# Kernel tuning notes

Measured on AMD Instinct MI355X. Metric: run time of the kernel, lower is better.

Reference implementation:

```python
import jax, jax.numpy as jnp
import numpy as np

N_NODES = 1_000_000
D_FEAT = 128
N_GRAPHS = 4096


def setup_inputs() -> dict:
    key = jax.random.key(0)
    k1, k2 = jax.random.split(key)
    feat = jax.random.normal(k1, (N_NODES, D_FEAT), dtype=jnp.float32)
    # per-node graph id (batched graph membership), sorted as in dgl.batch ordering
    segment_ids = jnp.sort(jax.random.randint(k2, (N_NODES,), 0, N_GRAPHS, dtype=jnp.int32))
    return {"feat": feat, "segment_ids": segment_ids, "num_segments": N_GRAPHS}


def reference(feat, segment_ids, num_segments):
    # Sum node features within each graph: [total_nodes, d] -> [num_graphs, d]
    return jax.ops.segment_sum(feat, segment_ids, num_segments=num_segments,
                               indices_are_sorted=True)
```

## Files before the change

### kernel.cpp

```cpp
#include <hip/hip_runtime.h>


#define D_FEAT 128
#define D4     32

typedef float f32x4 __attribute__((ext_vector_type(4)));

__global__ __launch_bounds__(256) void seg_offsets_kernel(
        const int* __restrict__ ids,
        int* __restrict__ offsets,
        int n_nodes, int num_segs) {
    int i = blockIdx.x * blockDim.x + threadIdx.x;
    if (i >= n_nodes) return;
    int cur  = ids[i];
    int prev = (i == 0) ? -1 : ids[i - 1];
    for (int s = prev + 1; s <= cur; ++s) offsets[s] = i;
    if (i == n_nodes - 1) {
        for (int s = cur + 1; s <= num_segs; ++s) offsets[s] = n_nodes;
    }
}

__global__ __launch_bounds__(256) void SumNode_11905649344609_kernel(
        const float* __restrict__ feat,
        const int* __restrict__ offsets,
        float* __restrict__ out) {
    const int seg   = blockIdx.x;
    const int start = offsets[seg];
    const int end   = offsets[seg + 1];

    const int tid  = threadIdx.x;
    const int c4   = tid & (D4 - 1);
    const int roff = tid >> 5;

    const f32x4* __restrict__ f4 = (const f32x4*)feat;

    f32x4 a0 = {0.f, 0.f, 0.f, 0.f};
    f32x4 a1 = a0, a2 = a0, a3 = a0;

    int r = start + roff;
    for (; r + 24 < end; r += 32) {
        f32x4 v0 = __builtin_nontemporal_load(&f4[(size_t)(r)      * D4 + c4]);
        f32x4 v1 = __builtin_nontemporal_load(&f4[(size_t)(r +  8) * D4 + c4]);
        f32x4 v2 = __builtin_nontemporal_load(&f4[(size_t)(r + 16) * D4 + c4]);
        f32x4 v3 = __builtin_nontemporal_load(&f4[(size_t)(r + 24) * D4 + c4]);
        a0 += v0; a1 += v1; a2 += v2; a3 += v3;
    }
    for (; r < end; r += 8) {
        a0 += __builtin_nontemporal_load(&f4[(size_t)r * D4 + c4]);
    }

    f32x4 acc = (a0 + a1) + (a2 + a3);

    __shared__ f32x4 sm[256];
    sm[tid] = acc;
    __syncthreads();
    if (tid < 128) sm[tid] += sm[tid + 128];
    __syncthreads();
    if (tid < 64)  sm[tid] += sm[tid + 64];
    __syncthreads();
    if (tid < 32) {
        f32x4 res = sm[tid] + sm[tid + 32];
        ((f32x4*)out)[(size_t)seg * D4 + tid] = res;
    }
}

extern "C" void kernel_launch(void* const* d_in, const int* in_sizes, int n_in,
                              void* d_out, int out_size, void* d_ws, size_t ws_size,
                              hipStream_t stream) {
    const float* feat = (const float*)d_in[0];
    const int*   ids  = (const int*)d_in[1];
    float*       out  = (float*)d_out;

    const int n_nodes  = in_sizes[1];
    const int num_segs = out_size / D_FEAT;

    int* offsets = (int*)d_ws;

    seg_offsets_kernel<<<(n_nodes + 255) / 256, 256, 0, stream>>>(
        ids, offsets, n_nodes, num_segs);
    SumNode_11905649344609_kernel<<<num_segs, 256, 0, stream>>>(feat, offsets, out);
}
```

Before: 616.3 us.

## Replace per-segment reduction with fixed-chunk scan and atomic flushes

Drops the offsets-building kernel and the one-block-per-segment reduction. Instead, each block handles a fixed chunk of 256 rows, and each thread keeps a running sum per segment id, flushing it to the zero-initialised output with float atomics whenever the id changes. This aims for even load balance and removes the offsets pass, but adds per-row id loads, a zeroing kernel, and many atomics, since every thread flushes separately (about 8 flushes per chunk column per segment). Summation order also becomes nondeterministic.

```diff
diff --git a/kernel.cpp b/kernel.cpp
--- a/kernel.cpp
+++ b/kernel.cpp
@@ -3,65 +3,74 @@
 
 #define D_FEAT 128
 #define D4     32
+#define CHUNK  256
 
 typedef float f32x4 __attribute__((ext_vector_type(4)));
 
-__global__ __launch_bounds__(256) void seg_offsets_kernel(
-        const int* __restrict__ ids,
-        int* __restrict__ offsets,
-        int n_nodes, int num_segs) {
+__global__ __launch_bounds__(256) void zero_out_kernel(
+        float* __restrict__ out, int n_f4) {
     int i = blockIdx.x * blockDim.x + threadIdx.x;
-    if (i >= n_nodes) return;
-    int cur  = ids[i];
-    int prev = (i == 0) ? -1 : ids[i - 1];
-    for (int s = prev + 1; s <= cur; ++s) offsets[s] = i;
-    if (i == n_nodes - 1) {
-        for (int s = cur + 1; s <= num_segs; ++s) offsets[s] = n_nodes;
+    if (i < n_f4) {
+        f32x4 z = {0.f, 0.f, 0.f, 0.f};
+        ((f32x4*)out)[i] = z;
     }
 }
 
 __global__ __launch_bounds__(256) void SumNode_11905649344609_kernel(
         const float* __restrict__ feat,
-        const int* __restrict__ offsets,
-        float* __restrict__ out) {
-    const int seg   = blockIdx.x;
-    const int start = offsets[seg];
-    const int end   = offsets[seg + 1];
-
+        const int* __restrict__ ids,
+        float* __restrict__ out,
+        int n_nodes) {
     const int tid  = threadIdx.x;
     const int c4   = tid & (D4 - 1);
     const int roff = tid >> 5;
 
+    const int base = blockIdx.x * CHUNK;
+    const int end  = (base + CHUNK < n_nodes) ? (base + CHUNK) : n_nodes;
+
     const f32x4* __restrict__ f4 = (const f32x4*)feat;
 
-    f32x4 a0 = {0.f, 0.f, 0.f, 0.f};
-    f32x4 a1 = a0, a2 = a0, a3 = a0;
+    f32x4 acc = {0.f, 0.f, 0.f, 0.f};
+    int   cur = -1;
 
-    int r = start + roff;
+    auto flush = [&]() {
+        if (cur >= 0) {
+            float* p = out + (size_t)cur * D_FEAT + c4 * 4;
+            unsafeAtomicAdd(p + 0, acc[0]);
+            unsafeAtomicAdd(p + 1, acc[1]);
+            unsafeAtomicAdd(p + 2, acc[2]);
+            unsafeAtomicAdd(p + 3, acc[3]);
+        }
+    };
+    auto proc = [&](int id, f32x4 v) {
+        if (__builtin_expect(id != cur, 0)) {
+            flush();
+            acc = (f32x4){0.f, 0.f, 0.f, 0.f};
+            cur = id;
+        }
+        acc += v;
+    };
+
+    int r = base + roff;
     for (; r + 24 < end; r += 32) {
         f32x4 v0 = __builtin_nontemporal_load(&f4[(size_t)(r)      * D4 + c4]);
         f32x4 v1 = __builtin_nontemporal_load(&f4[(size_t)(r +  8) * D4 + c4]);
         f32x4 v2 = __builtin_nontemporal_load(&f4[(size_t)(r + 16) * D4 + c4]);
         f32x4 v3 = __builtin_nontemporal_load(&f4[(size_t)(r + 24) * D4 + c4]);
-        a0 += v0; a1 += v1; a2 += v2; a3 += v3;
+        int i0 = ids[r];
+        int i1 = ids[r + 8];
+        int i2 = ids[r + 16];
+        int i3 = ids[r + 24];
+        proc(i0, v0);
+        proc(i1, v1);
+        proc(i2, v2);
+        proc(i3, v3);
     }
     for (; r < end; r += 8) {
-        a0 += __builtin_nontemporal_load(&f4[(size_t)r * D4 + c4]);
+        f32x4 v = __builtin_nontemporal_load(&f4[(size_t)r * D4 + c4]);
+        proc(ids[r], v);
     }
-
-    f32x4 acc = (a0 + a1) + (a2 + a3);
-
-    __shared__ f32x4 sm[256];
-    sm[tid] = acc;
-    __syncthreads();
-    if (tid < 128) sm[tid] += sm[tid + 128];
-    __syncthreads();
-    if (tid < 64)  sm[tid] += sm[tid + 64];
-    __syncthreads();
-    if (tid < 32) {
-        f32x4 res = sm[tid] + sm[tid + 32];
-        ((f32x4*)out)[(size_t)seg * D4 + tid] = res;
-    }
+    flush();
 }
 
 extern "C" void kernel_launch(void* const* d_in, const int* in_sizes, int n_in,
@@ -71,12 +80,12 @@
     const int*   ids  = (const int*)d_in[1];
     float*       out  = (float*)d_out;
 
-    const int n_nodes  = in_sizes[1];
-    const int num_segs = out_size / D_FEAT;
+    const int n_nodes = in_sizes[1];
+    const int n_f4    = out_size / 4;
 
-    int* offsets = (int*)d_ws;
+    zero_out_kernel<<<(n_f4 + 255) / 256, 256, 0, stream>>>(out, n_f4);
 
-    seg_offsets_kernel<<<(n_nodes + 255) / 256, 256, 0, stream>>>(
-        ids, offsets, n_nodes, num_segs);
-    SumNode_11905649344609_kernel<<<num_segs, 256, 0, stream>>>(feat, offsets, out);
+    const int n_chunks = (n_nodes + CHUNK - 1) / CHUNK;
+    SumNode_11905649344609_kernel<<<n_chunks, 256, 0, stream>>>(
+        feat, ids, out, n_nodes);
 }
```

After: 695.5 us. 1.13x slower.
